# Performance work log

Hardware: AMD Instinct MI355X
Metric: run time of the kernel (lower is better)

Reference implementation:

```python
import jax, jax.numpy as jnp
import numpy as np

B, T, E = 8, 2048, 512   # batch, tokens, embedding_dim
K, C = 8192, 8           # num_embeddings, codebook_dim
LN_EPS = 1e-5


def _layer_norm(x, g, b):
    mu = jnp.mean(x, axis=-1, keepdims=True)
    var = jnp.var(x, axis=-1, keepdims=True)
    return (x - mu) * jax.lax.rsqrt(var + LN_EPS) * g + b


def setup_inputs() -> dict:
    key = jax.random.key(0)
    ks = jax.random.split(key, 8)
    s_e = 1.0 / np.sqrt(E)
    s_c = 1.0 / np.sqrt(C)
    return {
        "features": jax.random.normal(ks[0], (B, T, E), dtype=jnp.float32),
        # project_in: Linear(E,E) -> ReLU -> Linear(E,C)
        "W1_in": jax.random.uniform(ks[1], (E, E), jnp.float32, -s_e, s_e),
        "b1_in": jnp.zeros((E,), jnp.float32),
        "W2_in": jax.random.uniform(ks[2], (E, C), jnp.float32, -s_e, s_e),
        "b2_in": jnp.zeros((C,), jnp.float32),
        "ln_in_g": jnp.ones((C,), jnp.float32),
        "ln_in_b": jnp.zeros((C,), jnp.float32),
        # codebook
        "emb": jax.random.normal(ks[3], (K, C), dtype=jnp.float32),
        # project_out: Linear(C,E) -> ReLU -> Linear(E,E)
        "W1_out": jax.random.uniform(ks[4], (C, E), jnp.float32, -s_c, s_c),
        "b1_out": jnp.zeros((E,), jnp.float32),
        "W2_out": jax.random.uniform(ks[5], (E, E), jnp.float32, -s_e, s_e),
        "b2_out": jnp.zeros((E,), jnp.float32),
        "ln_out_g": jnp.ones((E,), jnp.float32),
        "ln_out_b": jnp.zeros((E,), jnp.float32),
    }


def reference(features, W1_in, b1_in, W2_in, b2_in, ln_in_g, ln_in_b, emb,
              W1_out, b1_out, W2_out, b2_out, ln_out_g, ln_out_b):
    # project_in + norm_in
    h = jax.nn.relu(jnp.einsum('bte,ef->btf', features, W1_in) + b1_in)
    z = jnp.einsum('bte,ec->btc', h, W2_in) + b2_in          # (B,T,C)
    z = _layer_norm(z, ln_in_g, ln_in_b)
    zf = z.reshape(-1, C)                                     # (N,C)
    d = (jnp.sum(zf * zf, axis=1, keepdims=True)
         - 2.0 * zf @ emb.T
         + jnp.sum(emb * emb, axis=1)[None, :])               # (N,K)
    idx = jnp.argmin(d, axis=1)                               # (N,)
    encodings = jax.nn.one_hot(idx, K, dtype=zf.dtype)        # (N,K)
    quantized = emb[idx]                                      # gather == one_hot @ emb
    # project_out + norm_out
    q = jax.nn.relu(quantized @ W1_out + b1_out)
    q = q @ W2_out + b2_out
    q = _layer_norm(q, ln_out_g, ln_out_b)
    q = q.reshape(B, T, E)
    return q, idx[:, None], encodings
```

## Files before the change

### kernel.cpp

```cpp
#include <hip/hip_runtime.h>
#include <cstdint>
#include <cstddef>

#define N_TOK 16384
#define E_DIM 512
#define C_DIM 8
#define K_CODES 8192
#define LN_EPS 1e-5f

template<bool RELU>
__global__ __launch_bounds__(256) void gemm_bias(const float* __restrict__ A,
    const float* __restrict__ B, const float* __restrict__ bias,
    float* __restrict__ C, int M, int N, int K) {
  __shared__ float As[16][132];
  __shared__ float Bs[16][68];
  const int tid = threadIdx.x;
  const int m0 = blockIdx.y * 128;
  const int n0 = blockIdx.x * 64;
  const int tx = tid & 15;
  const int ty = tid >> 4;
  const int ar = tid >> 1;
  const int ak = (tid & 1) * 8;
  const int bk = tid >> 4;
  const int bn = (tid & 15) * 4;
  float acc[8][4];
#pragma unroll
  for (int i = 0; i < 8; ++i)
#pragma unroll
    for (int j = 0; j < 4; ++j) acc[i][j] = 0.f;

  for (int k0 = 0; k0 < K; k0 += 16) {
    const float* Ap = A + (size_t)(m0 + ar) * K + (k0 + ak);
    float4 a0 = *(const float4*)(Ap);
    float4 a1 = *(const float4*)(Ap + 4);
    const float* Bp = B + (size_t)(k0 + bk) * N + (n0 + bn);
    float4 b0 = *(const float4*)(Bp);
    __syncthreads();
    As[ak + 0][ar] = a0.x; As[ak + 1][ar] = a0.y; As[ak + 2][ar] = a0.z; As[ak + 3][ar] = a0.w;
    As[ak + 4][ar] = a1.x; As[ak + 5][ar] = a1.y; As[ak + 6][ar] = a1.z; As[ak + 7][ar] = a1.w;
    Bs[bk][bn + 0] = b0.x; Bs[bk][bn + 1] = b0.y; Bs[bk][bn + 2] = b0.z; Bs[bk][bn + 3] = b0.w;
    __syncthreads();
#pragma unroll
    for (int kk = 0; kk < 16; ++kk) {
      float a[8], b[4];
#pragma unroll
      for (int i = 0; i < 8; ++i) a[i] = As[kk][ty * 8 + i];
#pragma unroll
      for (int j = 0; j < 4; ++j) b[j] = Bs[kk][tx * 4 + j];
#pragma unroll
      for (int i = 0; i < 8; ++i)
#pragma unroll
        for (int j = 0; j < 4; ++j) acc[i][j] = fmaf(a[i], b[j], acc[i][j]);
    }
  }
  float4 bv = *(const float4*)(bias + n0 + tx * 4);
#pragma unroll
  for (int i = 0; i < 8; ++i) {
    float4 r;
    r.x = acc[i][0] + bv.x; r.y = acc[i][1] + bv.y;
    r.z = acc[i][2] + bv.z; r.w = acc[i][3] + bv.w;
    if (RELU) {
      r.x = fmaxf(r.x, 0.f); r.y = fmaxf(r.y, 0.f);
      r.z = fmaxf(r.z, 0.f); r.w = fmaxf(r.w, 0.f);
    }
    *(float4*)(C + (size_t)(m0 + ty * 8 + i) * N + n0 + tx * 4) = r;
  }
}

__global__ __launch_bounds__(256) void zln_kernel(const float* __restrict__ h,
    const float* __restrict__ W2, const float* __restrict__ b2,
    const float* __restrict__ g, const float* __restrict__ b,
    float* __restrict__ z) {
  int token = blockIdx.x * 4 + (threadIdx.x >> 6);
  int lane = threadIdx.x & 63;
  const float* hr = h + (size_t)token * E_DIM;
  float acc[C_DIM];
#pragma unroll
  for (int c = 0; c < C_DIM; ++c) acc[c] = 0.f;
  for (int e = lane; e < E_DIM; e += 64) {
    float hv = hr[e];
    const float* w = W2 + e * C_DIM;
#pragma unroll
    for (int c = 0; c < C_DIM; ++c) acc[c] = fmaf(hv, w[c], acc[c]);
  }
#pragma unroll
  for (int c = 0; c < C_DIM; ++c) {
#pragma unroll
    for (int off = 32; off > 0; off >>= 1) acc[c] += __shfl_down(acc[c], off);
  }
  if (lane == 0) {
    float v[C_DIM]; float mu = 0.f;
#pragma unroll
    for (int c = 0; c < C_DIM; ++c) { v[c] = acc[c] + b2[c]; mu += v[c]; }
    mu *= 0.125f;
    float var = 0.f;
#pragma unroll
    for (int c = 0; c < C_DIM; ++c) { float d = v[c] - mu; var += d * d; }
    var *= 0.125f;
    float inv = 1.0f / sqrtf(var + LN_EPS);
#pragma unroll
    for (int c = 0; c < C_DIM; ++c)
      z[(size_t)token * C_DIM + c] = ((v[c] - mu) * inv) * g[c] + b[c];
  }
}

__global__ void ne_kernel(const float* __restrict__ emb, float* __restrict__ ne) {
  int k = blockIdx.x * 256 + threadIdx.x;
  const float* e = emb + (size_t)k * C_DIM;
  float s = 0.f;
#pragma unroll
  for (int c = 0; c < C_DIM; ++c) s = fmaf(e[c], e[c], s);
  ne[k] = s;
}

__global__ __launch_bounds__(256) void vq_partial(const float* __restrict__ z,
    const float* __restrict__ emb, const float* __restrict__ ne,
    float* __restrict__ pbest, int* __restrict__ pidx) {
  int chunk = blockIdx.x & 7;
  int token = (blockIdx.x >> 3) * 256 + threadIdx.x;
  float zv[C_DIM];
#pragma unroll
  for (int c = 0; c < C_DIM; ++c) zv[c] = z[(size_t)token * C_DIM + c];
  float s = 0.f;
#pragma unroll
  for (int c = 0; c < C_DIM; ++c) s = fmaf(zv[c], zv[c], s);
  float best = 3.402823466e38f; int bi = 0;
  int j0 = chunk * 1024;
  for (int j = j0; j < j0 + 1024; ++j) {
    const float* e = emb + (size_t)j * C_DIM;
    float p = 0.f;
#pragma unroll
    for (int c = 0; c < C_DIM; ++c) p = fmaf(zv[c], e[c], p);
    float d = fmaf(-2.f, p, s) + ne[j];
    if (d < best) { best = d; bi = j; }
  }
  pbest[chunk * N_TOK + token] = best;
  pidx[chunk * N_TOK + token] = bi;
}

__global__ void vq_combine(const float* __restrict__ pbest, const int* __restrict__ pidx,
    int* __restrict__ idx_i, float* __restrict__ idxf) {
  int n = blockIdx.x * 256 + threadIdx.x;
  float best = pbest[n]; int bi = pidx[n];
#pragma unroll
  for (int c = 1; c < 8; ++c) {
    float bb = pbest[c * N_TOK + n]; int i2 = pidx[c * N_TOK + n];
    if (bb < best) { best = bb; bi = i2; }
  }
  idx_i[n] = bi;
  idxf[n] = (float)bi;
}

__global__ __launch_bounds__(128) void proj_out1(const float* __restrict__ emb,
    const float* __restrict__ W1, const float* __restrict__ b1, float* __restrict__ t) {
  int k = blockIdx.x;
  int e = threadIdx.x * 4;
  float4 acc = *(const float4*)(b1 + e);
#pragma unroll
  for (int c = 0; c < C_DIM; ++c) {
    float ev = emb[(size_t)k * C_DIM + c];
    float4 w = *(const float4*)(W1 + (size_t)c * E_DIM + e);
    acc.x = fmaf(ev, w.x, acc.x); acc.y = fmaf(ev, w.y, acc.y);
    acc.z = fmaf(ev, w.z, acc.z); acc.w = fmaf(ev, w.w, acc.w);
  }
  acc.x = fmaxf(acc.x, 0.f); acc.y = fmaxf(acc.y, 0.f);
  acc.z = fmaxf(acc.z, 0.f); acc.w = fmaxf(acc.w, 0.f);
  *(float4*)(t + (size_t)k * E_DIM + e) = acc;
}

__global__ __launch_bounds__(256) void ln512(float* __restrict__ g,
    const float* __restrict__ gw, const float* __restrict__ bw) {
  int row = blockIdx.x; int tid = threadIdx.x;
  float* r = g + (size_t)row * E_DIM;
  float v0 = r[tid], v1 = r[tid + 256];
  __shared__ float red[8];
  int lane = tid & 63, wid = tid >> 6;
  float sum = v0 + v1;
#pragma unroll
  for (int off = 32; off > 0; off >>= 1) sum += __shfl_xor(sum, off);
  if (lane == 0) red[wid] = sum;
  __syncthreads();
  float mu = (red[0] + red[1] + red[2] + red[3]) * (1.0f / 512.0f);
  float d0 = v0 - mu, d1 = v1 - mu;
  float sq = d0 * d0 + d1 * d1;
#pragma unroll
  for (int off = 32; off > 0; off >>= 1) sq += __shfl_xor(sq, off);
  if (lane == 0) red[4 + wid] = sq;
  __syncthreads();
  float var = (red[4] + red[5] + red[6] + red[7]) * (1.0f / 512.0f);
  float inv = 1.0f / sqrtf(var + LN_EPS);
  r[tid]       = (d0 * inv) * gw[tid] + bw[tid];
  r[tid + 256] = (d1 * inv) * gw[tid + 256] + bw[tid + 256];
}

__global__ __launch_bounds__(128) void out_gather(const float* __restrict__ oc,
    const int* __restrict__ idx_i, float* __restrict__ q) {
  int n = blockIdx.x;
  int k = idx_i[n];
  int e = threadIdx.x * 4;
  *(float4*)(q + (size_t)n * E_DIM + e) = *(const float4*)(oc + (size_t)k * E_DIM + e);
}

__global__ void scatter_ones(const float* __restrict__ idxf, float* __restrict__ enc) {
  int n = blockIdx.x * 256 + threadIdx.x;
  int k = (int)idxf[n];
  enc[(size_t)n * K_CODES + k] = 1.0f;
}

extern "C" void kernel_launch(void* const* d_in, const int* in_sizes, int n_in,
                              void* d_out, int out_size, void* d_ws, size_t ws_size,
                              hipStream_t stream) {
  const float* features = (const float*)d_in[0];
  const float* W1_in  = (const float*)d_in[1];
  const float* b1_in  = (const float*)d_in[2];
  const float* W2_in  = (const float*)d_in[3];
  const float* b2_in  = (const float*)d_in[4];
  const float* ln_in_g = (const float*)d_in[5];
  const float* ln_in_b = (const float*)d_in[6];
  const float* emb    = (const float*)d_in[7];
  const float* W1_out = (const float*)d_in[8];
  const float* b1_out = (const float*)d_in[9];
  const float* W2_out = (const float*)d_in[10];
  const float* b2_out = (const float*)d_in[11];
  const float* ln_out_g = (const float*)d_in[12];
  const float* ln_out_b = (const float*)d_in[13];

  float* q    = (float*)d_out;
  float* idxf = q + (size_t)N_TOK * E_DIM;
  float* enc  = idxf + N_TOK;

  float* h     = enc;
  float* t     = enc + 8388608;
  float* g     = enc + 12582912;
  float* z     = enc + 16777216;
  float* ne    = enc + 16908288;
  float* pbest = enc + 16916480;
  int*   idx_i = (int*)(enc + 17047552);
  int*   pidx  = (int*)(enc + 17063936);

  ne_kernel<<<K_CODES / 256, 256, 0, stream>>>(emb, ne);

  dim3 g1(E_DIM / 64, N_TOK / 128);
  gemm_bias<true><<<g1, 256, 0, stream>>>(features, W1_in, b1_in, h, N_TOK, E_DIM, E_DIM);

  zln_kernel<<<N_TOK / 4, 256, 0, stream>>>(h, W2_in, b2_in, ln_in_g, ln_in_b, z);

  vq_partial<<<(N_TOK / 256) * 8, 256, 0, stream>>>(z, emb, ne, pbest, pidx);
  vq_combine<<<N_TOK / 256, 256, 0, stream>>>(pbest, pidx, idx_i, idxf);

  proj_out1<<<K_CODES, 128, 0, stream>>>(emb, W1_out, b1_out, t);

  dim3 g2(E_DIM / 64, K_CODES / 128);
  gemm_bias<false><<<g2, 256, 0, stream>>>(t, W2_out, b2_out, g, K_CODES, E_DIM, E_DIM);

  ln512<<<K_CODES, 256, 0, stream>>>(g, ln_out_g, ln_out_b);

  out_gather<<<N_TOK, 128, 0, stream>>>(g, idx_i, q);

  hipMemsetAsync(enc, 0, (size_t)N_TOK * K_CODES * sizeof(float), stream);
  scatter_ones<<<N_TOK / 256, 256, 0, stream>>>(idxf, enc);
}
```

Before: 891.2 us.

## Spread encodings zero-fill across compute kernels instead of a trailing memset

The single large memset of the one-hot encodings buffer is removed. Each block of the two GEMMs, the VQ search and the output layer norm now zeroes its own slice of that buffer after finishing its compute. Each slice only covers memory whose scratch contents are no longer needed at that point, and a small final kernel clears the remaining scratch region. The aim is to hide the bandwidth-bound fill behind compute-bound phases. In exchange it adds tail work to those kernels, depends on careful offset bookkeeping over the aliased scratch, and may lengthen the kernels it is attached to.

```diff
diff --git a/kernel.cpp b/kernel.cpp
--- a/kernel.cpp
+++ b/kernel.cpp
@@ -8,10 +8,21 @@
 #define K_CODES 8192
 #define LN_EPS 1e-5f
 
+#define SCRATCH_END_F 17195008
+#define ENC_TOTAL_F   134217728
+#define UPPER_F4      ((ENC_TOTAL_F - SCRATCH_END_F) / 4)
+
+__device__ __forceinline__ void zero_slice(float4* zb, long start, int per, long ztotal) {
+  long cnt = ztotal - start; if (cnt > per) cnt = per; if (cnt < 0) cnt = 0;
+  float4 zero = make_float4(0.f, 0.f, 0.f, 0.f);
+  for (int i = threadIdx.x; i < (int)cnt; i += blockDim.x) zb[start + i] = zero;
+}
+
 template<bool RELU>
 __global__ __launch_bounds__(256) void gemm_bias(const float* __restrict__ A,
     const float* __restrict__ B, const float* __restrict__ bias,
-    float* __restrict__ C, int M, int N, int K) {
+    float* __restrict__ C, int M, int N, int K,
+    float4* __restrict__ zb, int zper, long ztotal) {
   __shared__ float As[16][132];
   __shared__ float Bs[16][68];
   const int tid = threadIdx.x;
@@ -65,6 +76,8 @@
     }
     *(float4*)(C + (size_t)(m0 + ty * 8 + i) * N + n0 + tx * 4) = r;
   }
+  long bid = (long)blockIdx.y * gridDim.x + blockIdx.x;
+  zero_slice(zb, bid * zper, zper, ztotal);
 }
 
 __global__ __launch_bounds__(256) void zln_kernel(const float* __restrict__ h,
@@ -115,7 +128,8 @@
 
 __global__ __launch_bounds__(256) void vq_partial(const float* __restrict__ z,
     const float* __restrict__ emb, const float* __restrict__ ne,
-    float* __restrict__ pbest, int* __restrict__ pidx) {
+    float* __restrict__ pbest, int* __restrict__ pidx,
+    float4* __restrict__ zb, int zper, long ztotal) {
   int chunk = blockIdx.x & 7;
   int token = (blockIdx.x >> 3) * 256 + threadIdx.x;
   float zv[C_DIM];
@@ -136,6 +150,7 @@
   }
   pbest[chunk * N_TOK + token] = best;
   pidx[chunk * N_TOK + token] = bi;
+  zero_slice(zb, (long)blockIdx.x * zper, zper, ztotal);
 }
 
 __global__ void vq_combine(const float* __restrict__ pbest, const int* __restrict__ pidx,
@@ -169,7 +184,8 @@
 }
 
 __global__ __launch_bounds__(256) void ln512(float* __restrict__ g,
-    const float* __restrict__ gw, const float* __restrict__ bw) {
+    const float* __restrict__ gw, const float* __restrict__ bw,
+    float4* __restrict__ zb, int zper, long ztotal) {
   int row = blockIdx.x; int tid = threadIdx.x;
   float* r = g + (size_t)row * E_DIM;
   float v0 = r[tid], v1 = r[tid + 256];
@@ -191,6 +207,7 @@
   float inv = 1.0f / sqrtf(var + LN_EPS);
   r[tid]       = (d0 * inv) * gw[tid] + bw[tid];
   r[tid + 256] = (d1 * inv) * gw[tid + 256] + bw[tid + 256];
+  zero_slice(zb, (long)blockIdx.x * zper, zper, ztotal);
 }
 
 __global__ __launch_bounds__(128) void out_gather(const float* __restrict__ oc,
@@ -199,6 +216,13 @@
   int k = idx_i[n];
   int e = threadIdx.x * 4;
   *(float4*)(q + (size_t)n * E_DIM + e) = *(const float4*)(oc + (size_t)k * E_DIM + e);
+}
+
+__global__ __launch_bounds__(256) void final_zero(float4* __restrict__ zb, long ztotal) {
+  float4 zero = make_float4(0.f, 0.f, 0.f, 0.f);
+  long stride = (long)gridDim.x * blockDim.x;
+  for (long i = (long)blockIdx.x * blockDim.x + threadIdx.x; i < ztotal; i += stride)
+    zb[i] = zero;
 }
 
 __global__ void scatter_ones(const float* __restrict__ idxf, float* __restrict__ enc) {
@@ -238,25 +262,36 @@
   int*   idx_i = (int*)(enc + 17047552);
   int*   pidx  = (int*)(enc + 17063936);
 
+  float4* upper = (float4*)(enc + SCRATCH_END_F);
+  long up_total = UPPER_F4;
+  long g1_base = 0;            int g1_per = 16384;
+  long g2_base = 16777216;     int g2_per = 12288;
+  long vq_base = 23068672;     int vq_per = 12288;
+
   ne_kernel<<<K_CODES / 256, 256, 0, stream>>>(emb, ne);
 
   dim3 g1(E_DIM / 64, N_TOK / 128);
-  gemm_bias<true><<<g1, 256, 0, stream>>>(features, W1_in, b1_in, h, N_TOK, E_DIM, E_DIM);
+  gemm_bias<true><<<g1, 256, 0, stream>>>(features, W1_in, b1_in, h, N_TOK, E_DIM, E_DIM,
+                                          upper + g1_base, g1_per, 16777216L);
 
   zln_kernel<<<N_TOK / 4, 256, 0, stream>>>(h, W2_in, b2_in, ln_in_g, ln_in_b, z);
 
-  vq_partial<<<(N_TOK / 256) * 8, 256, 0, stream>>>(z, emb, ne, pbest, pidx);
+  vq_partial<<<(N_TOK / 256) * 8, 256, 0, stream>>>(z, emb, ne, pbest, pidx,
+                                          upper + vq_base, vq_per, up_total - vq_base);
   vq_combine<<<N_TOK / 256, 256, 0, stream>>>(pbest, pidx, idx_i, idxf);
 
   proj_out1<<<K_CODES, 128, 0, stream>>>(emb, W1_out, b1_out, t);
 
   dim3 g2(E_DIM / 64, K_CODES / 128);
-  gemm_bias<false><<<g2, 256, 0, stream>>>(t, W2_out, b2_out, g, K_CODES, E_DIM, E_DIM);
-
-  ln512<<<K_CODES, 256, 0, stream>>>(g, ln_out_g, ln_out_b);
+  gemm_bias<false><<<g2, 256, 0, stream>>>(t, W2_out, b2_out, g, K_CODES, E_DIM, E_DIM,
+                                          upper + g2_base, g2_per, 6291456L);
+
+  ln512<<<K_CODES, 256, 0, stream>>>(g, ln_out_g, ln_out_b,
+                                     (float4*)enc, 384, 3145728L);
 
   out_gather<<<N_TOK, 128, 0, stream>>>(g, idx_i, q);
 
-  hipMemsetAsync(enc, 0, (size_t)N_TOK * K_CODES * sizeof(float), stream);
+  final_zero<<<512, 256, 0, stream>>>((float4*)(enc + 12582912), 1153024L);
+
   scatter_ones<<<N_TOK / 256, 256, 0, stream>>>(idxf, enc);
 }
```

Result: no change. 906.2 us (+1.7%).
